# Kernel optimization log

Measured on AMD Instinct MI355X. Metric: run time of the kernel, lower is better.

The kernel has to match this reference:

```python
import jax, jax.numpy as jnp
import numpy as np

N_NODES = 50000
N_EDGES = 800000
IN_DIM = 64
EDGE_DIM = 16
HID = 128
L = 3
G = 128  # number of graphs in the batch
EPS = 1e-5


def _glorot(key, shape):
    fan_in, fan_out = shape[0], shape[1]
    lim = float(np.sqrt(6.0 / (fan_in + fan_out)))
    return jax.random.uniform(key, shape, jnp.float32, -lim, lim)


def setup_inputs() -> dict:
    key = jax.random.key(0)
    ks = jax.random.split(key, 40)
    inp = {}
    inp["x"] = jax.random.uniform(ks[0], (N_NODES, IN_DIM), jnp.float32)
    inp["edge_index"] = jax.random.randint(ks[1], (2, N_EDGES), 0, N_NODES, jnp.int64)
    inp["edge_attr"] = jax.random.normal(ks[2], (N_EDGES, EDGE_DIM), jnp.float32)
    inp["batch"] = jnp.sort(jax.random.randint(ks[3], (N_NODES,), 0, G, jnp.int64))
    # ligand / protein input MLPs: Linear-ReLU-Linear-ReLU
    inp["lig_w1"] = _glorot(ks[4], (IN_DIM, HID)); inp["lig_b1"] = jnp.zeros((HID,), jnp.float32)
    inp["lig_w2"] = _glorot(ks[5], (HID, HID));    inp["lig_b2"] = jnp.zeros((HID,), jnp.float32)
    inp["prot_w1"] = _glorot(ks[6], (IN_DIM, HID)); inp["prot_b1"] = jnp.zeros((HID,), jnp.float32)
    inp["prot_w2"] = _glorot(ks[7], (HID, HID));    inp["prot_b2"] = jnp.zeros((HID,), jnp.float32)
    # per-layer GINEConv params (stacked over layers)
    inp["edge_w"] = jnp.stack([_glorot(ks[8 + i], (EDGE_DIM, HID)) for i in range(L)])
    inp["edge_b"] = jnp.zeros((L, HID), jnp.float32)
    inp["nn_w1"] = jnp.stack([_glorot(ks[12 + i], (HID, HID)) for i in range(L)])
    inp["nn_b1"] = jnp.zeros((L, HID), jnp.float32)
    inp["nn_w2"] = jnp.stack([_glorot(ks[16 + i], (HID, HID)) for i in range(L)])
    inp["nn_b2"] = jnp.zeros((L, HID), jnp.float32)
    # GraphNorm params: weight=1, bias=0, mean_scale=1
    inp["gn_w"] = jnp.ones((L, HID), jnp.float32)
    inp["gn_b"] = jnp.zeros((L, HID), jnp.float32)
    inp["gn_ms"] = jnp.ones((L, HID), jnp.float32)
    # output head: Linear-ReLU-Linear(1)
    inp["fc_w1"] = _glorot(ks[20], (HID, HID)); inp["fc_b1"] = jnp.zeros((HID,), jnp.float32)
    inp["fc_w2"] = _glorot(ks[21], (HID, 1));   inp["fc_b2"] = jnp.zeros((1,), jnp.float32)
    return inp


def reference(x, edge_index, edge_attr, batch,
              lig_w1, lig_b1, lig_w2, lig_b2,
              prot_w1, prot_b1, prot_w2, prot_b2,
              edge_w, edge_b, nn_w1, nn_b1, nn_w2, nn_b2,
              gn_w, gn_b, gn_ms,
              fc_w1, fc_b1, fc_w2, fc_b2):
    relu = lambda a: jnp.maximum(a, 0)
    src, dst = edge_index[0], edge_index[1]

    # input encoders, merged per node by protein flag (last feature column)
    is_prot = x[:, -1] > 0.5
    h_lig = relu(relu(x @ lig_w1 + lig_b1) @ lig_w2 + lig_b2)
    h_prot = relu(relu(x @ prot_w1 + prot_b1) @ prot_w2 + prot_b2)
    h = jnp.where(is_prot[:, None], h_prot, h_lig)

    # per-graph node counts for GraphNorm
    cnt = jax.ops.segment_sum(jnp.ones((x.shape[0],), jnp.float32), batch, num_segments=G)
    cnt = jnp.maximum(cnt, 1.0)[:, None]

    for l in range(L):
        # GINEConv (eps=0): out = nn(x + sum_{j->i} relu(x_j + lin(e_ji)))
        e = edge_attr @ edge_w[l] + edge_b[l]              # [E, HID]
        msg = relu(h[src] + e)                             # gather + add + relu
        aggr = jax.ops.segment_sum(msg, dst, num_segments=h.shape[0])
        h = aggr + h
        h = relu(h @ nn_w1[l] + nn_b1[l]) @ nn_w2[l] + nn_b2[l]
        # GraphNorm: per-graph mean/var with learnable mean_scale
        mean = jax.ops.segment_sum(h, batch, num_segments=G) / cnt
        hc = h - mean[batch] * gn_ms[l]
        var = jax.ops.segment_sum(hc * hc, batch, num_segments=G) / cnt
        h = gn_w[l] * hc * jax.lax.rsqrt(var[batch] + EPS) + gn_b[l]
        h = relu(h)  # (dropout=0.0 -> identity)

    g = jax.ops.segment_sum(h, batch, num_segments=G)      # global_add_pool
    out = relu(g @ fc_w1 + fc_b1) @ fc_w2 + fc_b2
    return out.reshape(-1)
```

## Files before the change

kernel.cpp:

```cpp
#include <hip/hip_runtime.h>

#define N_NODES 50000
#define N_EDGES 800000
#define IN_DIM  64
#define EDGE_DIM 16
#define HID     128
#define NLAYERS 3
#define NGRAPH  128
#define EPS     1e-5f

typedef __attribute__((ext_vector_type(8))) short bf8_t;
typedef __attribute__((ext_vector_type(4))) short bf4_t;
typedef __attribute__((ext_vector_type(4))) float f32x4;

__device__ __forceinline__ unsigned short f2bf(float x) {
    unsigned u = __float_as_uint(x);
    unsigned r = u + 0x7fffu + ((u >> 16) & 1u);
    return (unsigned short)(r >> 16);
}
__device__ __forceinline__ float bf2f(unsigned short v) {
    return __uint_as_float(((unsigned)v) << 16);
}

__global__ void k_init(int* __restrict__ row_cnt, float* __restrict__ pool,
                       float* __restrict__ gsum, float* __restrict__ gsq) {
    int i = blockIdx.x * blockDim.x + threadIdx.x;
    if (i < N_NODES) row_cnt[i] = 0;
    if (i < NGRAPH * HID) { pool[i] = 0.0f; gsum[i] = 0.0f; gsq[i] = 0.0f; }
}

__global__ __launch_bounds__(NGRAPH) void k_count(const int* __restrict__ batch,
                                                  float* __restrict__ cnt) {
    int g = threadIdx.x;
    int lo = 0, hi = N_NODES;
    while (lo < hi) { int mid = (lo + hi) >> 1; if (batch[mid] < g) lo = mid + 1; else hi = mid; }
    int a = lo;
    lo = 0; hi = N_NODES;
    while (lo < hi) { int mid = (lo + hi) >> 1; if (batch[mid] < g + 1) lo = mid + 1; else hi = mid; }
    cnt[g] = (float)(lo - a);
}

__global__ void k_wconv(const float* __restrict__ nw1, const float* __restrict__ nw2,
                        unsigned short* __restrict__ wt) {
    int idx = blockIdx.x * 256 + threadIdx.x;
    if (idx >= NLAYERS * 2 * HID * HID) return;
    int k = idx & 127;
    int n = (idx >> 7) & 127;
    int which = (idx >> 14) & 1;
    int l = idx >> 15;
    const float* w = (which == 0 ? nw1 : nw2) + l * HID * HID;
    wt[idx] = f2bf(w[k * HID + n]);
}

__global__ void k_wconv_enc(const float* __restrict__ lw1, const float* __restrict__ pw1,
                            const float* __restrict__ lw2, const float* __restrict__ pw2,
                            unsigned short* __restrict__ we) {
    int idx = blockIdx.x * 256 + threadIdx.x;
    if (idx >= 49152) return;
    float v;
    if (idx < 8192)       { int n = idx >> 6, k = idx & 63;            v = lw1[k * HID + n]; }
    else if (idx < 16384) { int r = idx - 8192;  int n = r >> 6, k = r & 63;  v = pw1[k * HID + n]; }
    else if (idx < 32768) { int r = idx - 16384; int n = r >> 7, k = r & 127; v = lw2[k * HID + n]; }
    else                  { int r = idx - 32768; int n = r >> 7, k = r & 127; v = pw2[k * HID + n]; }
    we[idx] = f2bf(v);
}

__global__ void k_wconv_e(const float* __restrict__ ew, const float* __restrict__ eb,
                          unsigned short* __restrict__ wte) {
    int idx = blockIdx.x * 256 + threadIdx.x;
    if (idx >= NLAYERS * 8 * 64 * 8) return;
    int j = idx & 7;
    int lane = (idx >> 3) & 63;
    int t = (idx >> 9) & 7;
    int l = idx >> 12;
    int k = (lane >> 4) * 8 + j;
    int feat = t * 16 + (lane & 15);
    float v = 0.0f;
    if (k < EDGE_DIM)       v = ew[l * EDGE_DIM * HID + k * HID + feat];
    else if (k == EDGE_DIM) v = eb[l * HID + feat];
    wte[idx] = f2bf(v);
}

__global__ void k_hist(const int* __restrict__ dsts, int* __restrict__ row_cnt) {
    int e = blockIdx.x * blockDim.x + threadIdx.x;
    if (e < N_EDGES) atomicAdd(&row_cnt[dsts[e]], 1);
}

__global__ __launch_bounds__(256) void k_scan1(const int* __restrict__ row_cnt,
                                               int* __restrict__ partial) {
    __shared__ int s[256];
    int t = threadIdx.x, b = blockIdx.x;
    int i0 = b * 512 + t;
    int v = 0;
    if (i0 < N_NODES) v += row_cnt[i0];
    if (i0 + 256 < N_NODES) v += row_cnt[i0 + 256];
    s[t] = v; __syncthreads();
    for (int off = 128; off > 0; off >>= 1) {
        if (t < off) s[t] += s[t + off];
        __syncthreads();
    }
    if (t == 0) partial[b] = s[0];
}

#define NCHUNK 98
__global__ __launch_bounds__(128) void k_scan2(int* __restrict__ partial) {
    __shared__ int s[128];
    int t = threadIdx.x;
    int v = (t < NCHUNK) ? partial[t] : 0;
    s[t] = v; __syncthreads();
    for (int off = 1; off < 128; off <<= 1) {
        int x = (t >= off) ? s[t - off] : 0;
        __syncthreads();
        s[t] += x;
        __syncthreads();
    }
    partial[t] = s[t] - v;
}

__global__ __launch_bounds__(512) void k_scan3(const int* __restrict__ row_cnt,
                                               const int* __restrict__ partial,
                                               int* __restrict__ row_start,
                                               int* __restrict__ row_fill) {
    __shared__ int s[512];
    int t = threadIdx.x, b = blockIdx.x;
    int i = b * 512 + t;
    int v = (i < N_NODES) ? row_cnt[i] : 0;
    s[t] = v; __syncthreads();
    for (int off = 1; off < 512; off <<= 1) {
        int x = (t >= off) ? s[t - off] : 0;
        __syncthreads();
        s[t] += x;
        __syncthreads();
    }
    int excl = s[t] - v + partial[b];
    if (i < N_NODES) { row_start[i] = excl; row_fill[i] = excl; }
}

__global__ void k_fill(const int* __restrict__ srcs, const int* __restrict__ dsts,
                       int* __restrict__ row_fill, int2* __restrict__ csr_se) {
    int e = blockIdx.x * blockDim.x + threadIdx.x;
    if (e < N_EDGES) {
        int p = atomicAdd(&row_fill[dsts[e]], 1);
        csr_se[p] = make_int2(srcs[e], e);
    }
}

__global__ __launch_bounds__(256) void k_reorder(const int2* __restrict__ csr_se,
                                                 const float* __restrict__ ea,
                                                 int* __restrict__ csr_src,
                                                 unsigned short* __restrict__ cea) {
    int p = blockIdx.x * blockDim.x + threadIdx.x;
    if (p < N_EDGES) {
        int2 se = csr_se[p];
        csr_src[p] = se.x;
        const float* s = ea + (size_t)se.y * EDGE_DIM;
        float4 a0 = *(const float4*)(s);
        float4 a1 = *(const float4*)(s + 4);
        float4 a2 = *(const float4*)(s + 8);
        float4 a3 = *(const float4*)(s + 12);
        bf8_t v0, v1;
        v0[0] = (short)f2bf(a0.x); v0[1] = (short)f2bf(a0.y);
        v0[2] = (short)f2bf(a0.z); v0[3] = (short)f2bf(a0.w);
        v0[4] = (short)f2bf(a1.x); v0[5] = (short)f2bf(a1.y);
        v0[6] = (short)f2bf(a1.z); v0[7] = (short)f2bf(a1.w);
        v1[0] = (short)f2bf(a2.x); v1[1] = (short)f2bf(a2.y);
        v1[2] = (short)f2bf(a2.z); v1[3] = (short)f2bf(a2.w);
        v1[4] = (short)f2bf(a3.x); v1[5] = (short)f2bf(a3.y);
        v1[6] = (short)f2bf(a3.z); v1[7] = (short)f2bf(a3.w);
        *(bf8_t*)(cea + (size_t)p * EDGE_DIM) = v0;
        *(bf8_t*)(cea + (size_t)p * EDGE_DIM + 8) = v1;
    }
}

#define HS 136
__global__ __launch_bounds__(256) void k_encoder_mfma(
    const float* __restrict__ x,
    const unsigned short* __restrict__ we,
    const float* __restrict__ lb1, const float* __restrict__ lb2,
    const float* __restrict__ pb1, const float* __restrict__ pb2,
    unsigned short* __restrict__ Hbp) {
    __shared__ short h1l[4 * 16 * HS];
    __shared__ short h1p[4 * 16 * HS];
    int w = threadIdx.x >> 6, lane = threadIdx.x & 63;
    int m = lane & 15, quad = lane >> 4;
    int nb = blockIdx.x * 64 + w * 16;
    short* hl = h1l + w * 16 * HS;
    short* hp = h1p + w * 16 * HS;
    int nclamp = nb + m; if (nclamp >= N_NODES) nclamp = N_NODES - 1;
    const float* xp = x + (size_t)nclamp * IN_DIM;

    f32x4 a1l[8], a1p[8];
    #pragma unroll
    for (int t = 0; t < 8; ++t) {
        float bl = lb1[t * 16 + m], bp = pb1[t * 16 + m];
        a1l[t] = (f32x4){bl, bl, bl, bl};
        a1p[t] = (f32x4){bp, bp, bp, bp};
    }
    #pragma unroll
    for (int s_ = 0; s_ < 2; ++s_) {
        int k0 = s_ * 32 + quad * 8;
        float4 a0 = *(const float4*)(xp + k0);
        float4 a1v = *(const float4*)(xp + k0 + 4);
        bf8_t af;
        af[0] = (short)f2bf(a0.x); af[1] = (short)f2bf(a0.y);
        af[2] = (short)f2bf(a0.z); af[3] = (short)f2bf(a0.w);
        af[4] = (short)f2bf(a1v.x); af[5] = (short)f2bf(a1v.y);
        af[6] = (short)f2bf(a1v.z); af[7] = (short)f2bf(a1v.w);
        #pragma unroll
        for (int t = 0; t < 8; ++t) {
            bf8_t bl = *(const bf8_t*)(we + (t * 16 + m) * 64 + k0);
            bf8_t bp = *(const bf8_t*)(we + 8192 + (t * 16 + m) * 64 + k0);
            a1l[t] = __builtin_amdgcn_mfma_f32_16x16x32_bf16(af, bl, a1l[t], 0, 0, 0);
            a1p[t] = __builtin_amdgcn_mfma_f32_16x16x32_bf16(af, bp, a1p[t], 0, 0, 0);
        }
    }
    #pragma unroll
    for (int t = 0; t < 8; ++t)
        #pragma unroll
        for (int r = 0; r < 4; ++r) {
            hl[(quad * 4 + r) * HS + t * 16 + m] = (short)f2bf(fmaxf(a1l[t][r], 0.0f));
            hp[(quad * 4 + r) * HS + t * 16 + m] = (short)f2bf(fmaxf(a1p[t][r], 0.0f));
        }
    __syncthreads();
    f32x4 a2l[8], a2p[8];
    #pragma unroll
    for (int t = 0; t < 8; ++t) {
        float bl = lb2[t * 16 + m], bp = pb2[t * 16 + m];
        a2l[t] = (f32x4){bl, bl, bl, bl};
        a2p[t] = (f32x4){bp, bp, bp, bp};
    }
    #pragma unroll
    for (int s_ = 0; s_ < 4; ++s_) {
        int k0 = s_ * 32 + quad * 8;
        bf8_t afl = *(const bf8_t*)(hl + m * HS + k0);
        bf8_t afp = *(const bf8_t*)(hp + m * HS + k0);
        #pragma unroll
        for (int t = 0; t < 8; ++t) {
            bf8_t bl = *(const bf8_t*)(we + 16384 + (t * 16 + m) * 128 + k0);
            bf8_t bp = *(const bf8_t*)(we + 32768 + (t * 16 + m) * 128 + k0);
            a2l[t] = __builtin_amdgcn_mfma_f32_16x16x32_bf16(afl, bl, a2l[t], 0, 0, 0);
            a2p[t] = __builtin_amdgcn_mfma_f32_16x16x32_bf16(afp, bp, a2p[t], 0, 0, 0);
        }
    }
    #pragma unroll
    for (int r = 0; r < 4; ++r) {
        int node = nb + quad * 4 + r;
        if (node < N_NODES) {
            float flg = x[(size_t)node * IN_DIM + (IN_DIM - 1)];
            bool prot = flg > 0.5f;
            bf8_t o;
            #pragma unroll
            for (int t = 0; t < 8; ++t) {
                float v = prot ? a2p[t][r] : a2l[t][r];
                o[t] = (short)f2bf(fmaxf(v, 0.0f));
            }
            *(bf8_t*)(Hbp + (size_t)node * HID + m * 8) = o;
        }
    }
}

__global__ __launch_bounds__(256, 8) void k_gather(
    const int* __restrict__ csr_src, const unsigned short* __restrict__ cea,
    const int* __restrict__ row_start, const int* __restrict__ row_end,
    const unsigned short* __restrict__ wte,
    const unsigned short* __restrict__ Hbp, unsigned short* __restrict__ Abp) {
    int w = threadIdx.x >> 6, lane = threadIdx.x & 63;
    int m = lane & 15, quad = lane >> 4;
    int n = blockIdx.x * 2 + (w >> 1);
    int half = w & 1;

    bf8_t bw[4];
    #pragma unroll
    for (int t = 0; t < 4; ++t)
        bw[t] = *(const bf8_t*)(wte + ((size_t)(half * 4 + t) * 64 + lane) * 8);

    float acc[4];
    #pragma unroll
    for (int t = 0; t < 4; ++t) acc[t] = 0.0f;

    int p  = __builtin_amdgcn_readfirstlane(row_start[n]);
    int pe = __builtin_amdgcn_readfirstlane(row_end[n]);

    const f32x4 zc = (f32x4){0.0f, 0.0f, 0.0f, 0.0f};

    for (; p + 16 <= pe; p += 16) {
        bf8_t af = (bf8_t){0, 0, 0, 0, 0, 0, 0, 0};
        if (quad < 2)
            af = *(const bf8_t*)(cea + (size_t)(p + m) * EDGE_DIM + quad * 8);
        else if (quad == 2)
            af[0] = (short)0x3F80;
        int sr[4];
        #pragma unroll
        for (int r = 0; r < 4; ++r) sr[r] = csr_src[p + quad * 4 + r];
        bf4_t hrow[4];
        #pragma unroll
        for (int r = 0; r < 4; ++r)
            hrow[r] = *(const bf4_t*)(Hbp + (size_t)sr[r] * HID + m * 8 + half * 4);
        f32x4 d[4];
        #pragma unroll
        for (int t = 0; t < 4; ++t)
            d[t] = __builtin_amdgcn_mfma_f32_16x16x32_bf16(af, bw[t], zc, 0, 0, 0);
        #pragma unroll
        for (int t = 0; t < 4; ++t)
            #pragma unroll
            for (int r = 0; r < 4; ++r)
                acc[t] += fmaxf(bf2f((unsigned short)hrow[r][t]) + d[t][r], 0.0f);
    }
    int rem = pe - p;
    if (rem > 0) {
        bf8_t af = (bf8_t){0, 0, 0, 0, 0, 0, 0, 0};
        if (quad < 2 && m < rem)
            af = *(const bf8_t*)(cea + (size_t)(p + m) * EDGE_DIM + quad * 8);
        else if (quad == 2)
            af[0] = (short)0x3F80;
        int sr[4];
        #pragma unroll
        for (int r = 0; r < 4; ++r) {
            int idx = p + quad * 4 + r; if (idx >= pe) idx = pe - 1;
            sr[r] = csr_src[idx];
        }
        bf4_t hrow[4];
        #pragma unroll
        for (int r = 0; r < 4; ++r)
            hrow[r] = *(const bf4_t*)(Hbp + (size_t)sr[r] * HID + m * 8 + half * 4);
        f32x4 d[4];
        #pragma unroll
        for (int t = 0; t < 4; ++t)
            d[t] = __builtin_amdgcn_mfma_f32_16x16x32_bf16(af, bw[t], zc, 0, 0, 0);
        #pragma unroll
        for (int t = 0; t < 4; ++t)
            #pragma unroll
            for (int r = 0; r < 4; ++r)
                if (quad * 4 + r < rem)
                    acc[t] += fmaxf(bf2f((unsigned short)hrow[r][t]) + d[t][r], 0.0f);
    }
    #pragma unroll
    for (int t = 0; t < 4; ++t) {
        acc[t] += __shfl_xor(acc[t], 16);
        acc[t] += __shfl_xor(acc[t], 32);
    }
    float asel = (quad == 0) ? acc[0] : (quad == 1) ? acc[1] : (quad == 2) ? acc[2] : acc[3];
    float self_ = bf2f(Hbp[(size_t)n * HID + m * 8 + half * 4 + quad]);
    Abp[(size_t)n * HID + (half * 4 + quad) * 16 + m] = f2bf(asel + self_);
}

#define MLP_NODES_PER_BLOCK 64
__global__ __launch_bounds__(256) void k_mlp_mfma(
    const unsigned short* __restrict__ Abp, const int* __restrict__ batch,
    const unsigned short* __restrict__ wt1, const unsigned short* __restrict__ wt2,
    const float* __restrict__ b1, const float* __restrict__ b2,
    float* __restrict__ H, float* __restrict__ gsum, float* __restrict__ gsq) {
    __shared__ short h1s[4 * 16 * HS];
    int w = threadIdx.x >> 6;
    int lane = threadIdx.x & 63;
    int m = lane & 15;
    int quad = lane >> 4;
    int nb = blockIdx.x * MLP_NODES_PER_BLOCK + w * 16;
    short* hw = h1s + w * 16 * HS;

    int nclamp = nb + m; if (nclamp >= N_NODES) nclamp = N_NODES - 1;
    const unsigned short* Ap = Abp + (size_t)nclamp * HID;
    f32x4 acc1[8];
    #pragma unroll
    for (int t = 0; t < 8; ++t) {
        float bv = b1[t * 16 + m];
        acc1[t] = (f32x4){bv, bv, bv, bv};
    }
    #pragma unroll
    for (int s_ = 0; s_ < 4; ++s_) {
        int k0 = s_ * 32 + quad * 8;
        bf8_t af = *(const bf8_t*)(Ap + k0);
        #pragma unroll
        for (int t = 0; t < 8; ++t) {
            bf8_t bf = *(const bf8_t*)(wt1 + (t * 16 + m) * HID + k0);
            acc1[t] = __builtin_amdgcn_mfma_f32_16x16x32_bf16(af, bf, acc1[t], 0, 0, 0);
        }
    }
    #pragma unroll
    for (int t = 0; t < 8; ++t)
        #pragma unroll
        for (int r = 0; r < 4; ++r) {
            float v = fmaxf(acc1[t][r], 0.0f);
            hw[(quad * 4 + r) * HS + t * 16 + m] = (short)f2bf(v);
        }
    __syncthreads();
    f32x4 acc2[8];
    #pragma unroll
    for (int t = 0; t < 8; ++t) {
        float bv = b2[t * 16 + m];
        acc2[t] = (f32x4){bv, bv, bv, bv};
    }
    #pragma unroll
    for (int s_ = 0; s_ < 4; ++s_) {
        int k0 = s_ * 32 + quad * 8;
        bf8_t af = *(const bf8_t*)(hw + m * HS + k0);
        #pragma unroll
        for (int t = 0; t < 8; ++t) {
            bf8_t bf = *(const bf8_t*)(wt2 + (t * 16 + m) * HID + k0);
            acc2[t] = __builtin_amdgcn_mfma_f32_16x16x32_bf16(af, bf, acc2[t], 0, 0, 0);
        }
    }
    #pragma unroll
    for (int t = 0; t < 8; ++t)
        #pragma unroll
        for (int r = 0; r < 4; ++r) {
            int node = nb + quad * 4 + r;
            if (node < N_NODES) H[(size_t)node * HID + t * 16 + m] = acc2[t][r];
        }
    int blast = nb + 15 < N_NODES ? batch[nb + 15] : -1;
    int g0 = batch[nb < N_NODES ? nb : N_NODES - 1];
    if (nb + 15 < N_NODES && g0 == blast) {
        #pragma unroll
        for (int t = 0; t < 8; ++t) {
            float s = 0.0f, q = 0.0f;
            #pragma unroll
            for (int r = 0; r < 4; ++r) { float v = acc2[t][r]; s += v; q += v * v; }
            s += __shfl_xor(s, 16); q += __shfl_xor(q, 16);
            s += __shfl_xor(s, 32); q += __shfl_xor(q, 32);
            if (quad == 0) {
                atomicAdd(&gsum[g0 * HID + t * 16 + m], s);
                atomicAdd(&gsq[g0 * HID + t * 16 + m], q);
            }
        }
    } else {
        #pragma unroll
        for (int t = 0; t < 8; ++t)
            #pragma unroll
            for (int r = 0; r < 4; ++r) {
                int node = nb + quad * 4 + r;
                if (node < N_NODES) {
                    int g = batch[node];
                    float v = acc2[t][r];
                    atomicAdd(&gsum[g * HID + t * 16 + m], v);
                    atomicAdd(&gsq[g * HID + t * 16 + m], v * v);
                }
            }
    }
}

__global__ __launch_bounds__(HID) void k_stats(
    float* __restrict__ gsum, float* __restrict__ gsq,
    const float* __restrict__ cnt,
    const float* __restrict__ gw, const float* __restrict__ gb,
    const float* __restrict__ gms,
    float* __restrict__ sc, float* __restrict__ of) {
    int g = blockIdx.x;
    int t = threadIdx.x;
    float c = fmaxf(cnt[g], 1.0f);
    float mean = gsum[g * HID + t] / c;
    float msq  = gsq[g * HID + t] / c;
    float ms = gms[t];
    float var = msq - mean * mean * ms * (2.0f - ms);
    var = fmaxf(var, 0.0f);
    float istd = rsqrtf(var + EPS);
    float s = gw[t] * istd;
    sc[g * HID + t] = s;
    of[g * HID + t] = gb[t] - s * mean * ms;
    gsum[g * HID + t] = 0.0f;
    gsq[g * HID + t]  = 0.0f;
}

#define NORM_N 8
__global__ __launch_bounds__(HID) void k_norm(
    const float* __restrict__ H, const int* __restrict__ batch,
    const float* __restrict__ sc, const float* __restrict__ of,
    unsigned short* __restrict__ Hbp, float* __restrict__ pool, int accumulate) {
    int n0 = blockIdx.x * NORM_N;
    int t = threadIdx.x;
    int m = t & 15, tt = t >> 4;
    int g0 = batch[n0], gN = batch[n0 + NORM_N - 1];
    if (g0 == gN) {
        float ssc = sc[g0 * HID + t], sof = of[g0 * HID + t];
        float ps = 0.0f;
        #pragma unroll
        for (int i = 0; i < NORM_N; ++i) {
            float v = fmaxf(H[(size_t)(n0 + i) * HID + t] * ssc + sof, 0.0f);
            Hbp[(size_t)(n0 + i) * HID + m * 8 + tt] = f2bf(v);
            ps += v;
        }
        if (accumulate) atomicAdd(&pool[g0 * HID + t], ps);
    } else {
        #pragma unroll
        for (int i = 0; i < NORM_N; ++i) {
            int g = batch[n0 + i];
            float v = fmaxf(H[(size_t)(n0 + i) * HID + t] * sc[g * HID + t] + of[g * HID + t], 0.0f);
            Hbp[(size_t)(n0 + i) * HID + m * 8 + tt] = f2bf(v);
            if (accumulate) atomicAdd(&pool[g * HID + t], v);
        }
    }
}

__global__ __launch_bounds__(HID) void k_head(
    const float* __restrict__ pool,
    const float* __restrict__ fw1, const float* __restrict__ fb1,
    const float* __restrict__ fw2, const float* __restrict__ fb2,
    float* __restrict__ out) {
    __shared__ float ps[HID];
    __shared__ float red[2];
    int g = blockIdx.x;
    int t = threadIdx.x;
    ps[t] = pool[g * HID + t];
    __syncthreads();
    float acc = fb1[t];
    #pragma unroll 4
    for (int k = 0; k < HID; ++k) acc = fmaf(ps[k], fw1[k * HID + t], acc);
    float p = fmaxf(acc, 0.0f) * fw2[t];
    #pragma unroll
    for (int off = 32; off > 0; off >>= 1) p += __shfl_down(p, off, 64);
    if ((t & 63) == 0) red[t >> 6] = p;
    __syncthreads();
    if (t == 0) out[g] = red[0] + red[1] + fb2[0];
}

extern "C" void kernel_launch(void* const* d_in, const int* in_sizes, int n_in,
                              void* d_out, int out_size, void* d_ws, size_t ws_size,
                              hipStream_t stream) {
    const float* x     = (const float*)d_in[0];
    const int*   ei    = (const int*)d_in[1];
    const float* ea    = (const float*)d_in[2];
    const int*   batch = (const int*)d_in[3];
    const float* lw1 = (const float*)d_in[4];
    const float* lb1 = (const float*)d_in[5];
    const float* lw2 = (const float*)d_in[6];
    const float* lb2 = (const float*)d_in[7];
    const float* pw1 = (const float*)d_in[8];
    const float* pb1 = (const float*)d_in[9];
    const float* pw2 = (const float*)d_in[10];
    const float* pb2 = (const float*)d_in[11];
    const float* ew  = (const float*)d_in[12];
    const float* eb  = (const float*)d_in[13];
    const float* nw1 = (const float*)d_in[14];
    const float* nb1 = (const float*)d_in[15];
    const float* nw2 = (const float*)d_in[16];
    const float* nb2 = (const float*)d_in[17];
    const float* gw  = (const float*)d_in[18];
    const float* gb  = (const float*)d_in[19];
    const float* gms = (const float*)d_in[20];
    const float* fw1 = (const float*)d_in[21];
    const float* fb1 = (const float*)d_in[22];
    const float* fw2 = (const float*)d_in[23];
    const float* fb2 = (const float*)d_in[24];
    float* out = (float*)d_out;

    float* ws   = (float*)d_ws;
    float* H    = ws;
    float* A    = H    + (size_t)N_NODES * HID;
    float* gsum = A    + (size_t)N_NODES * HID;
    float* gsq  = gsum + NGRAPH * HID;
    float* sc   = gsq  + NGRAPH * HID;
    float* of   = sc   + NGRAPH * HID;
    float* pool = of   + NGRAPH * HID;
    float* cnt  = pool + NGRAPH * HID;
    int* row_cnt   = (int*)(cnt + NGRAPH);
    int* row_start = row_cnt + N_NODES;
    int* row_fill  = row_start + N_NODES;
    int* partial   = row_fill + N_NODES;
    int* csr_src   = partial + 128;
    unsigned short* cea  = (unsigned short*)(csr_src + N_EDGES);
    unsigned short* wt   = cea + (size_t)N_EDGES * EDGE_DIM;
    unsigned short* wenc = wt + NLAYERS * 2 * HID * HID;
    unsigned short* wte  = wenc + 49152;
    unsigned short* Hbp  = wte + NLAYERS * 8 * 64 * 8;
    unsigned short* Abp  = (unsigned short*)A;
    int2* csr_se = (int2*)(Abp + (size_t)N_NODES * HID);

    const int* srcs = ei;
    const int* dsts = ei + N_EDGES;

    k_init<<<(N_NODES + 255) / 256, 256, 0, stream>>>(row_cnt, pool, gsum, gsq);
    k_count<<<1, NGRAPH, 0, stream>>>(batch, cnt);
    k_wconv<<<(NLAYERS * 2 * HID * HID + 255) / 256, 256, 0, stream>>>(nw1, nw2, wt);
    k_wconv_enc<<<(49152 + 255) / 256, 256, 0, stream>>>(lw1, pw1, lw2, pw2, wenc);
    k_wconv_e<<<(NLAYERS * 8 * 64 * 8 + 255) / 256, 256, 0, stream>>>(ew, eb, wte);
    k_hist<<<(N_EDGES + 255) / 256, 256, 0, stream>>>(dsts, row_cnt);
    k_scan1<<<NCHUNK, 256, 0, stream>>>(row_cnt, partial);
    k_scan2<<<1, 128, 0, stream>>>(partial);
    k_scan3<<<NCHUNK, 512, 0, stream>>>(row_cnt, partial, row_start, row_fill);
    k_fill<<<(N_EDGES + 255) / 256, 256, 0, stream>>>(srcs, dsts, row_fill, csr_se);
    k_reorder<<<(N_EDGES + 255) / 256, 256, 0, stream>>>(csr_se, ea, csr_src, cea);

    k_encoder_mfma<<<(N_NODES + 63) / 64, 256, 0, stream>>>(
        x, wenc, lb1, lb2, pb1, pb2, Hbp);

    int mlp_blocks = (N_NODES + MLP_NODES_PER_BLOCK - 1) / MLP_NODES_PER_BLOCK;
    for (int l = 0; l < NLAYERS; ++l) {
        k_gather<<<N_NODES / 2, 256, 0, stream>>>(
            csr_src, cea, row_start, row_fill,
            wte + (size_t)l * 4096, Hbp, Abp);
        k_mlp_mfma<<<mlp_blocks, 256, 0, stream>>>(
            Abp, batch,
            wt + (size_t)l * 2 * HID * HID,
            wt + (size_t)l * 2 * HID * HID + HID * HID,
            nb1 + l * HID, nb2 + l * HID, H, gsum, gsq);
        k_stats<<<NGRAPH, HID, 0, stream>>>(gsum, gsq, cnt,
                                            gw + l * HID, gb + l * HID, gms + l * HID,
                                            sc, of);
        k_norm<<<N_NODES / NORM_N, HID, 0, stream>>>(
            H, batch, sc, of, Hbp, pool, (l == NLAYERS - 1) ? 1 : 0);
    }
    k_head<<<NGRAPH, HID, 0, stream>>>(pool, fw1, fb1, fw2, fb2, out);
}
```

Measured before the change: 675.3 us.

## Store MLP output in bf16 and split encoder ligand/protein paths across waves

The MLP kernel now writes its pre-norm output as bf16 instead of fp32, and the norm kernel reads it back as bf16, halving that intermediate's write and read traffic per layer. The encoder is restructured so each wave computes either the ligand or the protein MLP for a 16-node tile, with 32 nodes per block and a higher occupancy hint, instead of every wave computing both branches. This cuts register pressure per wave. It also means only the matching branch writes each node. Rounding the MLP output to bf16 before GraphNorm adds precision loss. The statistics are still computed from the fp32 accumulators, so they may drift slightly from the values that get normalized.

```diff
diff --git a/kernel.cpp b/kernel.cpp
--- a/kernel.cpp
+++ b/kernel.cpp
@@ -173,28 +173,30 @@
 }
 
 #define HS 136
-__global__ __launch_bounds__(256) void k_encoder_mfma(
+__global__ __launch_bounds__(256, 8) void k_encoder_mfma(
     const float* __restrict__ x,
     const unsigned short* __restrict__ we,
     const float* __restrict__ lb1, const float* __restrict__ lb2,
     const float* __restrict__ pb1, const float* __restrict__ pb2,
     unsigned short* __restrict__ Hbp) {
-    __shared__ short h1l[4 * 16 * HS];
-    __shared__ short h1p[4 * 16 * HS];
+    __shared__ short h1s[4][16 * HS];
     int w = threadIdx.x >> 6, lane = threadIdx.x & 63;
     int m = lane & 15, quad = lane >> 4;
-    int nb = blockIdx.x * 64 + w * 16;
-    short* hl = h1l + w * 16 * HS;
-    short* hp = h1p + w * 16 * HS;
+    int tile = w >> 1, role = w & 1;
+    int nb = blockIdx.x * 32 + tile * 16;
+    short* hl = h1s[w];
     int nclamp = nb + m; if (nclamp >= N_NODES) nclamp = N_NODES - 1;
     const float* xp = x + (size_t)nclamp * IN_DIM;
-
-    f32x4 a1l[8], a1p[8];
+    const float* b1 = role ? pb1 : lb1;
+    const float* b2 = role ? pb2 : lb2;
+    const unsigned short* w1 = we + role * 8192;
+    const unsigned short* w2 = we + 16384 + role * 16384;
+
+    f32x4 a1[8];
     #pragma unroll
     for (int t = 0; t < 8; ++t) {
-        float bl = lb1[t * 16 + m], bp = pb1[t * 16 + m];
-        a1l[t] = (f32x4){bl, bl, bl, bl};
-        a1p[t] = (f32x4){bp, bp, bp, bp};
+        float bv = b1[t * 16 + m];
+        a1[t] = (f32x4){bv, bv, bv, bv};
     }
     #pragma unroll
     for (int s_ = 0; s_ < 2; ++s_) {
@@ -208,53 +210,44 @@
         af[6] = (short)f2bf(a1v.z); af[7] = (short)f2bf(a1v.w);
         #pragma unroll
         for (int t = 0; t < 8; ++t) {
-            bf8_t bl = *(const bf8_t*)(we + (t * 16 + m) * 64 + k0);
-            bf8_t bp = *(const bf8_t*)(we + 8192 + (t * 16 + m) * 64 + k0);
-            a1l[t] = __builtin_amdgcn_mfma_f32_16x16x32_bf16(af, bl, a1l[t], 0, 0, 0);
-            a1p[t] = __builtin_amdgcn_mfma_f32_16x16x32_bf16(af, bp, a1p[t], 0, 0, 0);
+            bf8_t bw = *(const bf8_t*)(w1 + (t * 16 + m) * 64 + k0);
+            a1[t] = __builtin_amdgcn_mfma_f32_16x16x32_bf16(af, bw, a1[t], 0, 0, 0);
         }
     }
     #pragma unroll
     for (int t = 0; t < 8; ++t)
         #pragma unroll
-        for (int r = 0; r < 4; ++r) {
-            hl[(quad * 4 + r) * HS + t * 16 + m] = (short)f2bf(fmaxf(a1l[t][r], 0.0f));
-            hp[(quad * 4 + r) * HS + t * 16 + m] = (short)f2bf(fmaxf(a1p[t][r], 0.0f));
-        }
+        for (int r = 0; r < 4; ++r)
+            hl[(quad * 4 + r) * HS + t * 16 + m] = (short)f2bf(fmaxf(a1[t][r], 0.0f));
     __syncthreads();
-    f32x4 a2l[8], a2p[8];
+    f32x4 a2[8];
     #pragma unroll
     for (int t = 0; t < 8; ++t) {
-        float bl = lb2[t * 16 + m], bp = pb2[t * 16 + m];
-        a2l[t] = (f32x4){bl, bl, bl, bl};
-        a2p[t] = (f32x4){bp, bp, bp, bp};
+        float bv = b2[t * 16 + m];
+        a2[t] = (f32x4){bv, bv, bv, bv};
     }
     #pragma unroll
     for (int s_ = 0; s_ < 4; ++s_) {
         int k0 = s_ * 32 + quad * 8;
-        bf8_t afl = *(const bf8_t*)(hl + m * HS + k0);
-        bf8_t afp = *(const bf8_t*)(hp + m * HS + k0);
+        bf8_t af = *(const bf8_t*)(hl + m * HS + k0);
         #pragma unroll
         for (int t = 0; t < 8; ++t) {
-            bf8_t bl = *(const bf8_t*)(we + 16384 + (t * 16 + m) * 128 + k0);
-            bf8_t bp = *(const bf8_t*)(we + 32768 + (t * 16 + m) * 128 + k0);
-            a2l[t] = __builtin_amdgcn_mfma_f32_16x16x32_bf16(afl, bl, a2l[t], 0, 0, 0);
-            a2p[t] = __builtin_amdgcn_mfma_f32_16x16x32_bf16(afp, bp, a2p[t], 0, 0, 0);
+            bf8_t bw = *(const bf8_t*)(w2 + (t * 16 + m) * 128 + k0);
+            a2[t] = __builtin_amdgcn_mfma_f32_16x16x32_bf16(af, bw, a2[t], 0, 0, 0);
         }
     }
     #pragma unroll
     for (int r = 0; r < 4; ++r) {
         int node = nb + quad * 4 + r;
         if (node < N_NODES) {
-            float flg = x[(size_t)node * IN_DIM + (IN_DIM - 1)];
-            bool prot = flg > 0.5f;
-            bf8_t o;
-            #pragma unroll
-            for (int t = 0; t < 8; ++t) {
-                float v = prot ? a2p[t][r] : a2l[t][r];
-                o[t] = (short)f2bf(fmaxf(v, 0.0f));
+            bool prot = x[(size_t)node * IN_DIM + (IN_DIM - 1)] > 0.5f;
+            if (prot == (role == 1)) {
+                bf8_t o;
+                #pragma unroll
+                for (int t = 0; t < 8; ++t)
+                    o[t] = (short)f2bf(fmaxf(a2[t][r], 0.0f));
+                *(bf8_t*)(Hbp + (size_t)node * HID + m * 8) = o;
             }
-            *(bf8_t*)(Hbp + (size_t)node * HID + m * 8) = o;
         }
     }
 }
@@ -349,7 +342,7 @@
     const unsigned short* __restrict__ Abp, const int* __restrict__ batch,
     const unsigned short* __restrict__ wt1, const unsigned short* __restrict__ wt2,
     const float* __restrict__ b1, const float* __restrict__ b2,
-    float* __restrict__ H, float* __restrict__ gsum, float* __restrict__ gsq) {
+    unsigned short* __restrict__ Hb, float* __restrict__ gsum, float* __restrict__ gsq) {
     __shared__ short h1s[4 * 16 * HS];
     int w = threadIdx.x >> 6;
     int lane = threadIdx.x & 63;
@@ -405,7 +398,7 @@
         #pragma unroll
         for (int r = 0; r < 4; ++r) {
             int node = nb + quad * 4 + r;
-            if (node < N_NODES) H[(size_t)node * HID + t * 16 + m] = acc2[t][r];
+            if (node < N_NODES) Hb[(size_t)node * HID + t * 16 + m] = f2bf(acc2[t][r]);
         }
     int blast = nb + 15 < N_NODES ? batch[nb + 15] : -1;
     int g0 = batch[nb < N_NODES ? nb : N_NODES - 1];
@@ -462,7 +455,7 @@
 
 #define NORM_N 8
 __global__ __launch_bounds__(HID) void k_norm(
-    const float* __restrict__ H, const int* __restrict__ batch,
+    const unsigned short* __restrict__ Hb, const int* __restrict__ batch,
     const float* __restrict__ sc, const float* __restrict__ of,
     unsigned short* __restrict__ Hbp, float* __restrict__ pool, int accumulate) {
     int n0 = blockIdx.x * NORM_N;
@@ -474,7 +467,7 @@
         float ps = 0.0f;
         #pragma unroll
         for (int i = 0; i < NORM_N; ++i) {
-            float v = fmaxf(H[(size_t)(n0 + i) * HID + t] * ssc + sof, 0.0f);
+            float v = fmaxf(bf2f(Hb[(size_t)(n0 + i) * HID + t]) * ssc + sof, 0.0f);
             Hbp[(size_t)(n0 + i) * HID + m * 8 + tt] = f2bf(v);
             ps += v;
         }
@@ -483,7 +476,7 @@
         #pragma unroll
         for (int i = 0; i < NORM_N; ++i) {
             int g = batch[n0 + i];
-            float v = fmaxf(H[(size_t)(n0 + i) * HID + t] * sc[g * HID + t] + of[g * HID + t], 0.0f);
+            float v = fmaxf(bf2f(Hb[(size_t)(n0 + i) * HID + t]) * sc[g * HID + t] + of[g * HID + t], 0.0f);
             Hbp[(size_t)(n0 + i) * HID + m * 8 + tt] = f2bf(v);
             if (accumulate) atomicAdd(&pool[g * HID + t], v);
         }
@@ -561,6 +554,7 @@
     unsigned short* wenc = wt + NLAYERS * 2 * HID * HID;
     unsigned short* wte  = wenc + 49152;
     unsigned short* Hbp  = wte + NLAYERS * 8 * 64 * 8;
+    unsigned short* Hb   = (unsigned short*)H;
     unsigned short* Abp  = (unsigned short*)A;
     int2* csr_se = (int2*)(Abp + (size_t)N_NODES * HID);
 
@@ -579,7 +573,7 @@
     k_fill<<<(N_EDGES + 255) / 256, 256, 0, stream>>>(srcs, dsts, row_fill, csr_se);
     k_reorder<<<(N_EDGES + 255) / 256, 256, 0, stream>>>(csr_se, ea, csr_src, cea);
 
-    k_encoder_mfma<<<(N_NODES + 63) / 64, 256, 0, stream>>>(
+    k_encoder_mfma<<<(N_NODES + 31) / 32, 256, 0, stream>>>(
         x, wenc, lb1, lb2, pb1, pb2, Hbp);
 
     int mlp_blocks = (N_NODES + MLP_NODES_PER_BLOCK - 1) / MLP_NODES_PER_BLOCK;
@@ -591,12 +585,12 @@
             Abp, batch,
             wt + (size_t)l * 2 * HID * HID,
             wt + (size_t)l * 2 * HID * HID + HID * HID,
-            nb1 + l * HID, nb2 + l * HID, H, gsum, gsq);
+            nb1 + l * HID, nb2 + l * HID, Hb, gsum, gsq);
         k_stats<<<NGRAPH, HID, 0, stream>>>(gsum, gsq, cnt,
                                             gw + l * HID, gb + l * HID, gms + l * HID,
                                             sc, of);
         k_norm<<<N_NODES / NORM_N, HID, 0, stream>>>(
-            H, batch, sc, of, Hbp, pool, (l == NLAYERS - 1) ? 1 : 0);
+            Hb, batch, sc, of, Hbp, pool, (l == NLAYERS - 1) ? 1 : 0);
     }
     k_head<<<NGRAPH, HID, 0, stream>>>(pool, fw1, fb1, fw2, fb2, out);
 }
```

Result: no change. 674.1 us (-0.2%).
